# Kernel optimization log

Measured on AMD Instinct MI355X. Metric: run time of the kernel, lower is better.

## Reference

```python
import jax, jax.numpy as jnp
import numpy as np

N = 169343        # ogbn-arxiv nodes
E_DIR = 2709488   # directed edges before symmetrization (avg degree ~16)
F_IN = 128
HID = 256
C = 40
ALPHA = 0.9       # propagation matrix is I - ALPHA * S (SPD, so CG converges)
TOL = 1e-5
MAXITER = 100
EPS = 1e-5        # haiku LayerNorm default eps


def _layernorm_axis0(x, scale, offset):
    # hk.LayerNorm(0, True, True): stats over the node axis, per-feature params
    mu = jnp.mean(x, axis=0, keepdims=True)
    var = jnp.mean(jnp.square(x - mu), axis=0, keepdims=True)
    return scale * (x - mu) * jax.lax.rsqrt(var + EPS) + offset


def setup_inputs() -> dict:
    key = jax.random.key(0)
    ks = jax.random.split(key, 8)
    src = jax.random.randint(ks[0], (E_DIR,), 0, N)
    dst = jax.random.randint(ks[1], (E_DIR,), 0, N)
    # symmetrize so S is symmetric -> I - ALPHA*S is SPD
    senders = jnp.concatenate([src, dst])
    receivers = jnp.concatenate([dst, src])
    deg = jnp.maximum(jnp.zeros((N,), jnp.float32).at[receivers].add(1.0), 1.0)
    edge_weights = jax.lax.rsqrt(deg[senders] * deg[receivers])  # D^-1/2 A D^-1/2
    node_features = jax.random.normal(ks[2], (N, F_IN), jnp.float32)

    def dense(k, fin, fout):
        return jax.random.normal(k, (fin, fout), jnp.float32) / np.sqrt(fin).astype(np.float32)

    return {
        "node_features": node_features,
        "senders": senders,
        "receivers": receivers,
        "edge_weights": edge_weights,
        "W0": dense(ks[3], F_IN, HID), "b0": jnp.zeros((HID,), jnp.float32),
        "g0": jnp.ones((HID,), jnp.float32), "o0": jnp.zeros((HID,), jnp.float32),
        "W1": dense(ks[4], HID, HID), "b1": jnp.zeros((HID,), jnp.float32),
        "g1": jnp.ones((HID,), jnp.float32), "o1": jnp.zeros((HID,), jnp.float32),
        "W2": dense(ks[5], HID, C), "b2": jnp.zeros((C,), jnp.float32),
        "is_training": False,
    }


def reference(node_features, senders, receivers, edge_weights,
              W0, b0, g0, o0, W1, b1, g1, o1, W2, b2, is_training):
    # MLP stack (dropout is identity since is_training=False / eval mode)
    h = jax.nn.relu(_layernorm_axis0(node_features @ W0 + b0, g0, o0))  # [N, HID]
    h = jax.nn.relu(_layernorm_axis0(h @ W1 + b1, g1, o1))              # [N, HID]
    logits = h @ W2 + b2                                                # [N, C]

    def matvec(x):  # (I - ALPHA * S) @ x, sparse via edge list
        msg = edge_weights[:, None] * x[senders]                        # [2E, C]
        return x - ALPHA * jax.ops.segment_sum(msg, receivers, num_segments=N)

    out, _ = jax.scipy.sparse.linalg.cg(matvec, logits, tol=TOL, maxiter=MAXITER)
    return out
```

## Files before the change

kernel.cpp:

```cpp
#include <hip/hip_runtime.h>
#include <hip/hip_fp16.h>

#define FIN   128
#define HIDN  256
#define CDIM  40
#define NITER 9
#define RB    2048
#define NBSH  10
#define NBMAX 256
#define CHUNK 8192
#define BSTRIDE 36864

typedef _Float16 h8 __attribute__((ext_vector_type(8)));
typedef float f4 __attribute__((ext_vector_type(4)));


__device__ __forceinline__ float block_reduce_256(float v, float* red) {
  const int t = threadIdx.x;
  __syncthreads();
  red[t] = v;
  __syncthreads();
#pragma unroll
  for (int o = 128; o > 0; o >>= 1) {
    if (t < o) red[t] += red[t + o];
    __syncthreads();
  }
  return red[0];
}

__device__ __forceinline__ unsigned pack_half2(float a, float b) {
  __half2 h = __floats2half2_rn(a, b);
  return *reinterpret_cast<unsigned*>(&h);
}


__global__ void zero_i32(int* __restrict__ a, int n) {
  int i = blockIdx.x * blockDim.x + threadIdx.x;
  int s = gridDim.x * blockDim.x;
  for (; i < n; i += s) a[i] = 0;
}

__global__ __launch_bounds__(256) void csr_binA(
    const int* __restrict__ send, const int* __restrict__ recv,
    const float* __restrict__ ew, uint2* __restrict__ staged,
    int* __restrict__ bcnt, int nbuck, int E2) {
  __shared__ int hist[NBMAX];
  __shared__ int offs[NBMAX];
  const int tid = threadIdx.x;
  const int c0 = blockIdx.x * CHUNK;
  const int ce = min(c0 + CHUNK, E2);
  for (int j = tid; j < nbuck; j += 256) hist[j] = 0;
  __syncthreads();
  for (int e = c0 + tid; e < ce; e += 256) atomicAdd(&hist[recv[e] >> NBSH], 1);
  __syncthreads();
  for (int j = tid; j < nbuck; j += 256)
    offs[j] = hist[j] ? atomicAdd(&bcnt[j], hist[j]) : 0;
  __syncthreads();
  for (int j = tid; j < nbuck; j += 256) hist[j] = 0;
  __syncthreads();
  for (int e = c0 + tid; e < ce; e += 256) {
    int rnode = recv[e];
    int b = rnode >> NBSH;
    int p = atomicAdd(&hist[b], 1);
    int idx = offs[b] + p;
    if (idx < BSTRIDE) {
      unsigned meta = ((unsigned)(rnode & 1023) << 18) | (unsigned)send[e];
      staged[(size_t)b * BSTRIDE + idx] = make_uint2(meta, __float_as_uint(ew[e]));
    }
  }
}

__global__ __launch_bounds__(256) void csr_bucket_scan(const int* __restrict__ bcnt,
                                                       int* __restrict__ bbase,
                                                       int* __restrict__ rowp,
                                                       int nbuck, int Nn) {
  __shared__ int lb[NBMAX];
  const int tid = threadIdx.x;
  for (int j = tid; j < nbuck; j += 256) lb[j] = bcnt[j];
  __syncthreads();
  if (tid == 0) {
    int base = 0;
    for (int b = 0; b < nbuck; ++b) { int c = lb[b]; lb[b] = base; base += c; }
    rowp[Nn] = base;
  }
  __syncthreads();
  for (int j = tid; j < nbuck; j += 256) bbase[j] = lb[j];
}

__global__ __launch_bounds__(256) void csr_passB(
    const uint2* __restrict__ staged, const int* __restrict__ bcnt,
    const int* __restrict__ bbase, int* __restrict__ rowp,
    int2* __restrict__ ecsr, int Nn) {
  __shared__ int cnt[1024];
  __shared__ int part[256];
  const int tid = threadIdx.x;
  const int b = blockIdx.x;
  const int n0 = b << NBSH;
  const int nn = min(1024, Nn - n0);
  const int cntE = bcnt[b];
  const size_t sbase = (size_t)b * BSTRIDE;
  const int fbase = bbase[b];
  for (int j = tid; j < 1024; j += 256) cnt[j] = 0;
  __syncthreads();
  for (int e = tid; e < cntE; e += 256) {
    unsigned meta = staged[sbase + e].x;
    atomicAdd(&cnt[meta >> 18], 1);
  }
  __syncthreads();
  const int b4 = tid * 4;
  int c0 = cnt[b4], c1 = cnt[b4 + 1], c2 = cnt[b4 + 2], c3 = cnt[b4 + 3];
  part[tid] = c0 + c1 + c2 + c3;
  __syncthreads();
  for (int o = 1; o < 256; o <<= 1) {
    int v = (tid >= o) ? part[tid - o] : 0;
    __syncthreads();
    part[tid] += v;
    __syncthreads();
  }
  int pre = (tid == 0) ? 0 : part[tid - 1];
  cnt[b4] = pre;
  cnt[b4 + 1] = pre + c0;
  cnt[b4 + 2] = pre + c0 + c1;
  cnt[b4 + 3] = pre + c0 + c1 + c2;
  __syncthreads();
  for (int j = tid; j < nn; j += 256) rowp[n0 + j] = fbase + cnt[j];
  __syncthreads();
  for (int e = tid; e < cntE; e += 256) {
    uint2 rec = staged[sbase + e];
    int rlow = rec.x >> 18;
    int col = rec.x & 0x3FFFF;
    int pos = atomicAdd(&cnt[rlow], 1);
    ecsr[fbase + pos] = make_int2(col, (int)rec.y);
  }
}


__global__ __launch_bounds__(256) void wconv(const float* __restrict__ w0,
                                             const float* __restrict__ w1,
                                             const float* __restrict__ w2,
                                             _Float16* __restrict__ out,
                                             int n0, int n1, int n2) {
  int i = blockIdx.x * 256 + threadIdx.x;
  int s = gridDim.x * 256;
  int tot = n0 + n1 + n2;
  for (; i < tot; i += s) {
    float v = (i < n0) ? w0[i] : (i < n0 + n1) ? w1[i - n0] : w2[i - n0 - n1];
    out[i] = (_Float16)v;
  }
}


template <bool AF32, bool LNA, bool STATS, bool INITCG>
__global__ __launch_bounds__(256) void gemm_mfma(
    const void* __restrict__ Avoid, const _Float16* __restrict__ Wh,
    const float* __restrict__ bias, const float* __restrict__ lnS,
    const float* __restrict__ lnT, void* __restrict__ Cvoid,
    float* __restrict__ statp,
    float* __restrict__ rP, float* __restrict__ pP,
    __half* __restrict__ phP, float* __restrict__ xP,
    float* __restrict__ rsp,
    int M, int K, int Nn) {
  __shared__ _Float16 As[128][40];
  __shared__ _Float16 Bs[64][40];
  __shared__ _Float16 sSh[256];
  __shared__ _Float16 sTh[256];
  __shared__ float sred[4][2][64];
  __shared__ float red[256];
  const int tid = threadIdx.x;
  if (LNA) {
    if (tid < K) { sSh[tid] = (_Float16)lnS[tid]; sTh[tid] = (_Float16)lnT[tid]; }
  }
  const int w = tid >> 6, l = tid & 63;
  const int lm = l & 15;
  const int lk = (l >> 4) * 8;
  const int lr4 = (l >> 4) * 4;
  const int arow = tid >> 1, acol = (tid & 1) * 16;
  const int bn = tid & 63, bk = (tid >> 6) * 8;
  const int rowBase = blockIdx.x * 128;
  const int n0 = blockIdx.y * 64;
  const int gr = rowBase + arow;
  const int gn = n0 + bn;
  f4 acc[2][4];
#pragma unroll
  for (int mi = 0; mi < 2; ++mi)
#pragma unroll
    for (int ni = 0; ni < 4; ++ni) {
      acc[mi][ni][0] = 0.f; acc[mi][ni][1] = 0.f;
      acc[mi][ni][2] = 0.f; acc[mi][ni][3] = 0.f;
    }

  for (int k0 = 0; k0 < K; k0 += 32) {
    h8 a0, a1;
    if (gr < M) {
      if (AF32) {
        const f4* ap = reinterpret_cast<const f4*>(
            (const float*)Avoid + (size_t)gr * K + k0 + acol);
#pragma unroll
        for (int v4 = 0; v4 < 2; ++v4) {
          f4 vv = ap[v4];
#pragma unroll
          for (int j = 0; j < 4; ++j) a0[v4 * 4 + j] = (_Float16)vv[j];
        }
#pragma unroll
        for (int v4 = 2; v4 < 4; ++v4) {
          f4 vv = ap[v4];
#pragma unroll
          for (int j = 0; j < 4; ++j) a1[(v4 - 2) * 4 + j] = (_Float16)vv[j];
        }
      } else {
        const h8* ap = reinterpret_cast<const h8*>(
            (const _Float16*)Avoid + (size_t)gr * K + k0 + acol);
        a0 = ap[0];
        a1 = ap[1];
      }
    } else {
#pragma unroll
      for (int j = 0; j < 8; ++j) { a0[j] = (_Float16)0.f; a1[j] = (_Float16)0.f; }
    }
    h8 hb;
#pragma unroll
    for (int j = 0; j < 8; ++j)
      hb[j] = (gn < Nn) ? Wh[(size_t)(k0 + bk + j) * Nn + gn] : (_Float16)0.f;

    __syncthreads();
    if (LNA) {
      h8 s0 = *reinterpret_cast<const h8*>(&sSh[k0 + acol]);
      h8 s1 = *reinterpret_cast<const h8*>(&sSh[k0 + acol + 8]);
      h8 t0 = *reinterpret_cast<const h8*>(&sTh[k0 + acol]);
      h8 t1 = *reinterpret_cast<const h8*>(&sTh[k0 + acol + 8]);
      a0 = a0 * s0 + t0;
      a1 = a1 * s1 + t1;
#pragma unroll
      for (int j = 0; j < 8; ++j) {
        a0[j] = a0[j] > (_Float16)0.f ? a0[j] : (_Float16)0.f;
        a1[j] = a1[j] > (_Float16)0.f ? a1[j] : (_Float16)0.f;
      }
    }
    *reinterpret_cast<h8*>(&As[arow][acol]) = a0;
    *reinterpret_cast<h8*>(&As[arow][acol + 8]) = a1;
    *reinterpret_cast<h8*>(&Bs[bn][bk]) = hb;
    __syncthreads();

    h8 bf[4];
#pragma unroll
    for (int ni = 0; ni < 4; ++ni)
      bf[ni] = *reinterpret_cast<const h8*>(&Bs[ni * 16 + lm][lk]);
#pragma unroll
    for (int mi = 0; mi < 2; ++mi) {
      h8 af = *reinterpret_cast<const h8*>(&As[w * 32 + mi * 16 + lm][lk]);
#pragma unroll
      for (int ni = 0; ni < 4; ++ni)
        acc[mi][ni] = __builtin_amdgcn_mfma_f32_16x16x32_f16(af, bf[ni], acc[mi][ni],
                                                             0, 0, 0);
    }
  }

  float sN[4] = {0.f, 0.f, 0.f, 0.f};
  float s2N[4] = {0.f, 0.f, 0.f, 0.f};
  float rsacc = 0.f;
#pragma unroll
  for (int mi = 0; mi < 2; ++mi)
#pragma unroll
    for (int ni = 0; ni < 4; ++ni) {
      int col = n0 + ni * 16 + lm;
      if (col >= Nn) continue;
      float bb = bias[col];
#pragma unroll
      for (int r = 0; r < 4; ++r) {
        int row = rowBase + w * 32 + mi * 16 + lr4 + r;
        if (row >= M) continue;
        float v = acc[mi][ni][r] + bb;
        if (INITCG) {
          size_t idx = (size_t)row * Nn + col;
          rP[idx] = v;
          pP[idx] = v;
          xP[idx] = 0.f;
          phP[(size_t)row * 64 + col] = __float2half(v);
          rsacc = fmaf(v, v, rsacc);
        } else {
          ((_Float16*)Cvoid)[(size_t)row * Nn + col] = (_Float16)v;
        }
        if (STATS) {
          sN[ni] += v;
          s2N[ni] = fmaf(v, v, s2N[ni]);
        }
      }
    }

  if (STATS) {
#pragma unroll
    for (int ni = 0; ni < 4; ++ni) {
      sN[ni] += __shfl_xor(sN[ni], 16);
      sN[ni] += __shfl_xor(sN[ni], 32);
      s2N[ni] += __shfl_xor(s2N[ni], 16);
      s2N[ni] += __shfl_xor(s2N[ni], 32);
    }
    __syncthreads();
    if (l < 16) {
#pragma unroll
      for (int ni = 0; ni < 4; ++ni) {
        sred[w][0][ni * 16 + l] = sN[ni];
        sred[w][1][ni * 16 + l] = s2N[ni];
      }
    }
    __syncthreads();
    if (tid < 64) {
      float t0 = sred[0][0][tid] + sred[1][0][tid] + sred[2][0][tid] + sred[3][0][tid];
      float t1 = sred[0][1][tid] + sred[1][1][tid] + sred[2][1][tid] + sred[3][1][tid];
      statp[(size_t)blockIdx.x * 512 + n0 + tid] = t0;
      statp[(size_t)blockIdx.x * 512 + 256 + n0 + tid] = t1;
    }
  }

  if (INITCG) {
    for (int idx = tid; idx < 128 * 6; idx += 256) {
      int row = rowBase + idx / 6;
      int ck = idx % 6;
      if (row < M) {
        uint2* dst = reinterpret_cast<uint2*>(phP + (size_t)row * 64 + 40) + ck;
        *dst = make_uint2(0u, 0u);
      }
    }
    float bs = block_reduce_256(rsacc, red);
    if (tid == 0) rsp[blockIdx.x] = bs;
  }
}


__global__ __launch_bounds__(256) void stats_final(const float* __restrict__ part,
                                                   const float* __restrict__ g,
                                                   const float* __restrict__ o,
                                                   float* __restrict__ lnS,
                                                   float* __restrict__ lnT,
                                                   int nblk, int M) {
  __shared__ float red[256];
  const int col = blockIdx.x;
  float s = 0.f, s2 = 0.f;
  for (int b = threadIdx.x; b < nblk; b += 256) {
    s += part[(size_t)b * 512 + col];
    s2 += part[(size_t)b * 512 + 256 + col];
  }
  float ts = block_reduce_256(s, red);
  float ts2 = block_reduce_256(s2, red);
  if (threadIdx.x == 0) {
    float invM = 1.f / (float)M;
    float mean = ts * invM;
    float var = fmaxf(ts2 * invM - mean * mean, 0.f);
    float rstd = rsqrtf(var + 1e-5f);
    float sc = g[col] * rstd;
    lnS[col] = sc;
    lnT[col] = o[col] - mean * sc;
  }
}

__global__ __launch_bounds__(256) void reduce_rs(const float* __restrict__ rs_p,
                                                 float* __restrict__ rsbuf, int count) {
  __shared__ float red[256];
  float s = 0.f;
  for (int i = threadIdx.x; i < count; i += 256) s += rs_p[i];
  float t = block_reduce_256(s, red);
  if (threadIdx.x == 0) rsbuf[0] = t;
}


__global__ __launch_bounds__(256) void cg_matvec(const float* __restrict__ p,
                                                 const __half* __restrict__ ph,
                                                 float* __restrict__ q,
                                                 const int* __restrict__ rowp,
                                                 const int2* __restrict__ ecsr,
                                                 float* __restrict__ pqp,
                                                 float* __restrict__ qqp, int N) {
  __shared__ float red[256];
  const int lane = threadIdx.x & 63;
  const int wid = threadIdx.x >> 6;
  const bool act = lane < CDIM;
  float pqacc = 0.f, qqacc = 0.f;
  for (int i = blockIdx.x * 4 + wid; i < N; i += gridDim.x * 4) {
    int beg = rowp[i], end = rowp[i + 1];
    float a0 = 0.f, a1 = 0.f, a2 = 0.f, a3 = 0.f;
    int e = beg;
    for (; e + 8 <= end; e += 8) {
      int2 e0 = ecsr[e],     e1 = ecsr[e + 1], e2 = ecsr[e + 2], e3 = ecsr[e + 3];
      int2 e4 = ecsr[e + 4], e5 = ecsr[e + 5], e6 = ecsr[e + 6], e7 = ecsr[e + 7];
      if (act) {
        a0 = fmaf(__int_as_float(e0.y), __half2float(ph[(size_t)e0.x * 64 + lane]), a0);
        a1 = fmaf(__int_as_float(e1.y), __half2float(ph[(size_t)e1.x * 64 + lane]), a1);
        a2 = fmaf(__int_as_float(e2.y), __half2float(ph[(size_t)e2.x * 64 + lane]), a2);
        a3 = fmaf(__int_as_float(e3.y), __half2float(ph[(size_t)e3.x * 64 + lane]), a3);
        a0 = fmaf(__int_as_float(e4.y), __half2float(ph[(size_t)e4.x * 64 + lane]), a0);
        a1 = fmaf(__int_as_float(e5.y), __half2float(ph[(size_t)e5.x * 64 + lane]), a1);
        a2 = fmaf(__int_as_float(e6.y), __half2float(ph[(size_t)e6.x * 64 + lane]), a2);
        a3 = fmaf(__int_as_float(e7.y), __half2float(ph[(size_t)e7.x * 64 + lane]), a3);
      }
    }
    for (; e + 4 <= end; e += 4) {
      int2 e0 = ecsr[e], e1 = ecsr[e + 1], e2 = ecsr[e + 2], e3 = ecsr[e + 3];
      if (act) {
        a0 = fmaf(__int_as_float(e0.y), __half2float(ph[(size_t)e0.x * 64 + lane]), a0);
        a1 = fmaf(__int_as_float(e1.y), __half2float(ph[(size_t)e1.x * 64 + lane]), a1);
        a2 = fmaf(__int_as_float(e2.y), __half2float(ph[(size_t)e2.x * 64 + lane]), a2);
        a3 = fmaf(__int_as_float(e3.y), __half2float(ph[(size_t)e3.x * 64 + lane]), a3);
      }
    }
    for (; e < end; ++e) {
      int2 e0 = ecsr[e];
      if (act)
        a0 = fmaf(__int_as_float(e0.y), __half2float(ph[(size_t)e0.x * 64 + lane]), a0);
    }
    if (act) {
      float pvv = p[(size_t)i * CDIM + lane];
      float qvv = fmaf(-0.9f, (a0 + a1) + (a2 + a3), pvv);
      q[(size_t)i * CDIM + lane] = qvv;
      pqacc = fmaf(pvv, qvv, pqacc);
      qqacc = fmaf(qvv, qvv, qqacc);
    }
  }
  float s1 = block_reduce_256(pqacc, red);
  float s2 = block_reduce_256(qqacc, red);
  if (threadIdx.x == 0) { pqp[blockIdx.x] = s1; qqp[blockIdx.x] = s2; }
}

__global__ __launch_bounds__(256) void cg_fused(float4* __restrict__ x,
                                                float4* __restrict__ r,
                                                float4* __restrict__ p,
                                                const float4* __restrict__ q,
                                                __half* __restrict__ ph,
                                                const float* __restrict__ pqp,
                                                const float* __restrict__ qqp,
                                                const float* __restrict__ rs_in,
                                                float* __restrict__ rs_out, int total4) {
  __shared__ float red[256];
  float s1 = 0.f, s2 = 0.f;
  for (int i = threadIdx.x; i < RB; i += 256) {
    s1 += pqp[i];
    s2 += qqp[i];
  }
  float pq = block_reduce_256(s1, red);
  float qq = block_reduce_256(s2, red);
  float rsold = *rs_in;
  float alpha = (pq > 0.f) ? (rsold / pq) : 0.f;
  float rsnew = fmaxf(fmaf(alpha * alpha, qq, -rsold), 0.f);
  float beta = (rsold > 0.f) ? (rsnew / rsold) : 0.f;
  if (threadIdx.x == 0) *rs_out = rsnew;
  for (int j = blockIdx.x * 256 + threadIdx.x; j < total4; j += gridDim.x * 256) {
    const int node = j / 10;
    const int qx = j - node * 10;
    float4 pv4 = p[j], qv4 = q[j], xv4 = x[j], rv4 = r[j];
    xv4.x = fmaf(alpha, pv4.x, xv4.x);
    xv4.y = fmaf(alpha, pv4.y, xv4.y);
    xv4.z = fmaf(alpha, pv4.z, xv4.z);
    xv4.w = fmaf(alpha, pv4.w, xv4.w);
    rv4.x = fmaf(-alpha, qv4.x, rv4.x);
    rv4.y = fmaf(-alpha, qv4.y, rv4.y);
    rv4.z = fmaf(-alpha, qv4.z, rv4.z);
    rv4.w = fmaf(-alpha, qv4.w, rv4.w);
    float4 pn;
    pn.x = fmaf(beta, pv4.x, rv4.x);
    pn.y = fmaf(beta, pv4.y, rv4.y);
    pn.z = fmaf(beta, pv4.z, rv4.z);
    pn.w = fmaf(beta, pv4.w, rv4.w);
    x[j] = xv4;
    r[j] = rv4;
    p[j] = pn;
    unsigned* dst = reinterpret_cast<unsigned*>(ph + (size_t)node * 64 + qx * 4);
    dst[0] = pack_half2(pn.x, pn.y);
    dst[1] = pack_half2(pn.z, pn.w);
  }
}


extern "C" void kernel_launch(void* const* d_in, const int* in_sizes, int n_in,
                              void* d_out, int out_size, void* d_ws, size_t ws_size,
                              hipStream_t stream) {
  const float* X   = (const float*)d_in[0];
  const int* send  = (const int*)d_in[1];
  const int* recv  = (const int*)d_in[2];
  const float* ew  = (const float*)d_in[3];
  const float* W0  = (const float*)d_in[4];
  const float* b0  = (const float*)d_in[5];
  const float* g0  = (const float*)d_in[6];
  const float* o0  = (const float*)d_in[7];
  const float* W1  = (const float*)d_in[8];
  const float* b1  = (const float*)d_in[9];
  const float* g1  = (const float*)d_in[10];
  const float* o1  = (const float*)d_in[11];
  const float* W2  = (const float*)d_in[12];
  const float* b2  = (const float*)d_in[13];

  const int N = in_sizes[0] / FIN;
  const int E2 = in_sizes[1];
  const int total = N * CDIM;
  const int total4 = total / 4;
  const int gm = (N + 127) / 128;
  const int nbuck = (N + 1023) >> NBSH;
  const int nw0 = FIN * HIDN, nw1 = HIDN * HIDN, nw2 = HIDN * CDIM;

  char* base = (char*)d_ws;
  size_t off = 0;
  auto carve = [&](size_t bytes) -> void* {
    void* ptr = base + off;
    off += (bytes + 255) & ~(size_t)255;
    return ptr;
  };
  int* rowp      = (int*)carve((size_t)(N + 1) * 4);
  int2* ecsr     = (int2*)carve((size_t)E2 * 8);
  _Float16* Y0h  = (_Float16*)carve((size_t)N * HIDN * 2);
  _Float16* Y1h  = (_Float16*)carve((size_t)N * HIDN * 2);
  float* statp   = (float*)carve((size_t)gm * 512 * 4);
  float* lnS0    = (float*)carve(256 * 4);
  float* lnT0    = (float*)carve(256 * 4);
  float* lnS1    = (float*)carve(256 * 4);
  float* lnT1    = (float*)carve(256 * 4);
  float* pqp     = (float*)carve((size_t)RB * 4);
  float* qqp     = (float*)carve((size_t)RB * 4);
  float* rsp     = (float*)carve((size_t)gm * 4);
  float* rsbuf   = (float*)carve(2 * 4);
  int* bcnt      = (int*)carve((size_t)nbuck * 4);
  int* bbase     = (int*)carve((size_t)nbuck * 4);
  _Float16* Whb  = (_Float16*)carve((size_t)(nw0 + nw1 + nw2) * 2);
  (void)n_in; (void)out_size;

  if (off > ws_size) return;
  if (nbuck > NBMAX) return;

  _Float16* Wh0 = Whb;
  _Float16* Wh1 = Whb + nw0;
  _Float16* Wh2 = Whb + nw0 + nw1;

  uint2* staged = (uint2*)Y0h;
  float* rv = (float*)Y0h;
  float* pv = rv + (size_t)total;
  float* qv = rv + (size_t)2 * total;
  __half* ph = (__half*)Y1h;
  float* xv = (float*)d_out;

  zero_i32<<<1, 256, 0, stream>>>(bcnt, nbuck);
  wconv<<<64, 256, 0, stream>>>(W0, W1, W2, Whb, nw0, nw1, nw2);
  const int nchunk = (E2 + CHUNK - 1) / CHUNK;
  csr_binA<<<nchunk, 256, 0, stream>>>(send, recv, ew, staged, bcnt, nbuck, E2);
  csr_bucket_scan<<<1, 256, 0, stream>>>(bcnt, bbase, rowp, nbuck, N);
  csr_passB<<<nbuck, 256, 0, stream>>>(staged, bcnt, bbase, rowp, ecsr, N);

  gemm_mfma<true, false, true, false><<<dim3(gm, HIDN / 64), 256, 0, stream>>>(
      X, Wh0, b0, nullptr, nullptr, Y0h, statp,
      nullptr, nullptr, nullptr, nullptr, nullptr, N, FIN, HIDN);
  stats_final<<<HIDN, 256, 0, stream>>>(statp, g0, o0, lnS0, lnT0, gm, N);
  gemm_mfma<false, true, true, false><<<dim3(gm, HIDN / 64), 256, 0, stream>>>(
      Y0h, Wh1, b1, lnS0, lnT0, Y1h, statp,
      nullptr, nullptr, nullptr, nullptr, nullptr, N, HIDN, HIDN);
  stats_final<<<HIDN, 256, 0, stream>>>(statp, g1, o1, lnS1, lnT1, gm, N);
  gemm_mfma<false, true, false, true><<<dim3(gm, 1), 256, 0, stream>>>(
      Y1h, Wh2, b2, lnS1, lnT1, nullptr, nullptr,
      rv, pv, ph, xv, rsp, N, HIDN, CDIM);
  reduce_rs<<<1, 256, 0, stream>>>(rsp, rsbuf, gm);

  for (int it = 0; it < NITER; ++it) {
    cg_matvec<<<RB, 256, 0, stream>>>(pv, ph, qv, rowp, ecsr, pqp, qqp, N);
    cg_fused<<<RB, 256, 0, stream>>>((float4*)xv, (float4*)rv, (float4*)pv,
                                     (const float4*)qv, ph, pqp, qqp,
                                     &rsbuf[it & 1], &rsbuf[(it + 1) & 1], total4);
  }
}
```

Baseline: 2.077 ms.

## Split half-precision search direction into 32+8 planes and drop fp32 p copy

The CG direction vector p is no longer kept in fp32. Only an fp16 copy remains, and it is stored as two compact arrays: 32 columns per row and 8 columns per row, replacing the padded 64-wide layout. The matvec gathers read 80 bytes per node instead of touching 128-byte padded rows, and the fused update no longer reads and writes an fp32 p. This also removes the padding-zero stores. The catch is that p is now kept only in fp16, so the x and beta updates use rounded p, which may loosen CG accuracy.

```diff
diff --git a/kernel.cpp b/kernel.cpp
--- a/kernel.cpp
+++ b/kernel.cpp
@@ -156,8 +156,8 @@
     const float* __restrict__ bias, const float* __restrict__ lnS,
     const float* __restrict__ lnT, void* __restrict__ Cvoid,
     float* __restrict__ statp,
-    float* __restrict__ rP, float* __restrict__ pP,
-    __half* __restrict__ phP, float* __restrict__ xP,
+    float* __restrict__ rP, __half* __restrict__ ph32P,
+    __half* __restrict__ ph8P, float* __restrict__ xP,
     float* __restrict__ rsp,
     int M, int K, int Nn) {
   __shared__ _Float16 As[128][40];
@@ -273,9 +273,9 @@
         if (INITCG) {
           size_t idx = (size_t)row * Nn + col;
           rP[idx] = v;
-          pP[idx] = v;
           xP[idx] = 0.f;
-          phP[(size_t)row * 64 + col] = __float2half(v);
+          if (col < 32) ph32P[(size_t)row * 32 + col] = __float2half(v);
+          else          ph8P[(size_t)row * 8 + col - 32] = __float2half(v);
           rsacc = fmaf(v, v, rsacc);
         } else {
           ((_Float16*)Cvoid)[(size_t)row * Nn + col] = (_Float16)v;
@@ -313,14 +313,6 @@
   }
 
   if (INITCG) {
-    for (int idx = tid; idx < 128 * 6; idx += 256) {
-      int row = rowBase + idx / 6;
-      int ck = idx % 6;
-      if (row < M) {
-        uint2* dst = reinterpret_cast<uint2*>(phP + (size_t)row * 64 + 40) + ck;
-        *dst = make_uint2(0u, 0u);
-      }
-    }
     float bs = block_reduce_256(rsacc, red);
     if (tid == 0) rsp[blockIdx.x] = bs;
   }
@@ -363,8 +355,8 @@
 }
 
 
-__global__ __launch_bounds__(256) void cg_matvec(const float* __restrict__ p,
-                                                 const __half* __restrict__ ph,
+__global__ __launch_bounds__(256) void cg_matvec(const __half* __restrict__ ph32,
+                                                 const __half* __restrict__ ph8,
                                                  float* __restrict__ q,
                                                  const int* __restrict__ rowp,
                                                  const int2* __restrict__ ecsr,
@@ -374,6 +366,8 @@
   const int lane = threadIdx.x & 63;
   const int wid = threadIdx.x >> 6;
   const bool act = lane < CDIM;
+  const __half* gb = (lane < 32) ? ph32 : (ph8 - 32);
+  const size_t gs = (lane < 32) ? 32 : 8;
   float pqacc = 0.f, qqacc = 0.f;
   for (int i = blockIdx.x * 4 + wid; i < N; i += gridDim.x * 4) {
     int beg = rowp[i], end = rowp[i + 1];
@@ -383,32 +377,32 @@
       int2 e0 = ecsr[e],     e1 = ecsr[e + 1], e2 = ecsr[e + 2], e3 = ecsr[e + 3];
       int2 e4 = ecsr[e + 4], e5 = ecsr[e + 5], e6 = ecsr[e + 6], e7 = ecsr[e + 7];
       if (act) {
-        a0 = fmaf(__int_as_float(e0.y), __half2float(ph[(size_t)e0.x * 64 + lane]), a0);
-        a1 = fmaf(__int_as_float(e1.y), __half2float(ph[(size_t)e1.x * 64 + lane]), a1);
-        a2 = fmaf(__int_as_float(e2.y), __half2float(ph[(size_t)e2.x * 64 + lane]), a2);
-        a3 = fmaf(__int_as_float(e3.y), __half2float(ph[(size_t)e3.x * 64 + lane]), a3);
-        a0 = fmaf(__int_as_float(e4.y), __half2float(ph[(size_t)e4.x * 64 + lane]), a0);
-        a1 = fmaf(__int_as_float(e5.y), __half2float(ph[(size_t)e5.x * 64 + lane]), a1);
-        a2 = fmaf(__int_as_float(e6.y), __half2float(ph[(size_t)e6.x * 64 + lane]), a2);
-        a3 = fmaf(__int_as_float(e7.y), __half2float(ph[(size_t)e7.x * 64 + lane]), a3);
+        a0 = fmaf(__int_as_float(e0.y), __half2float(gb[(size_t)e0.x * gs + lane]), a0);
+        a1 = fmaf(__int_as_float(e1.y), __half2float(gb[(size_t)e1.x * gs + lane]), a1);
+        a2 = fmaf(__int_as_float(e2.y), __half2float(gb[(size_t)e2.x * gs + lane]), a2);
+        a3 = fmaf(__int_as_float(e3.y), __half2float(gb[(size_t)e3.x * gs + lane]), a3);
+        a0 = fmaf(__int_as_float(e4.y), __half2float(gb[(size_t)e4.x * gs + lane]), a0);
+        a1 = fmaf(__int_as_float(e5.y), __half2float(gb[(size_t)e5.x * gs + lane]), a1);
+        a2 = fmaf(__int_as_float(e6.y), __half2float(gb[(size_t)e6.x * gs + lane]), a2);
+        a3 = fmaf(__int_as_float(e7.y), __half2float(gb[(size_t)e7.x * gs + lane]), a3);
       }
     }
     for (; e + 4 <= end; e += 4) {
       int2 e0 = ecsr[e], e1 = ecsr[e + 1], e2 = ecsr[e + 2], e3 = ecsr[e + 3];
       if (act) {
-        a0 = fmaf(__int_as_float(e0.y), __half2float(ph[(size_t)e0.x * 64 + lane]), a0);
-        a1 = fmaf(__int_as_float(e1.y), __half2float(ph[(size_t)e1.x * 64 + lane]), a1);
-        a2 = fmaf(__int_as_float(e2.y), __half2float(ph[(size_t)e2.x * 64 + lane]), a2);
-        a3 = fmaf(__int_as_float(e3.y), __half2float(ph[(size_t)e3.x * 64 + lane]), a3);
+        a0 = fmaf(__int_as_float(e0.y), __half2float(gb[(size_t)e0.x * gs + lane]), a0);
+        a1 = fmaf(__int_as_float(e1.y), __half2float(gb[(size_t)e1.x * gs + lane]), a1);
+        a2 = fmaf(__int_as_float(e2.y), __half2float(gb[(size_t)e2.x * gs + lane]), a2);
+        a3 = fmaf(__int_as_float(e3.y), __half2float(gb[(size_t)e3.x * gs + lane]), a3);
       }
     }
     for (; e < end; ++e) {
       int2 e0 = ecsr[e];
       if (act)
-        a0 = fmaf(__int_as_float(e0.y), __half2float(ph[(size_t)e0.x * 64 + lane]), a0);
+        a0 = fmaf(__int_as_float(e0.y), __half2float(gb[(size_t)e0.x * gs + lane]), a0);
     }
     if (act) {
-      float pvv = p[(size_t)i * CDIM + lane];
+      float pvv = __half2float(gb[(size_t)i * gs + lane]);
       float qvv = fmaf(-0.9f, (a0 + a1) + (a2 + a3), pvv);
       q[(size_t)i * CDIM + lane] = qvv;
       pqacc = fmaf(pvv, qvv, pqacc);
@@ -422,9 +416,9 @@
 
 __global__ __launch_bounds__(256) void cg_fused(float4* __restrict__ x,
                                                 float4* __restrict__ r,
-                                                float4* __restrict__ p,
                                                 const float4* __restrict__ q,
-                                                __half* __restrict__ ph,
+                                                __half* __restrict__ ph32,
+                                                __half* __restrict__ ph8,
                                                 const float* __restrict__ pqp,
                                                 const float* __restrict__ qqp,
                                                 const float* __restrict__ rs_in,
@@ -445,26 +439,33 @@
   for (int j = blockIdx.x * 256 + threadIdx.x; j < total4; j += gridDim.x * 256) {
     const int node = j / 10;
     const int qx = j - node * 10;
-    float4 pv4 = p[j], qv4 = q[j], xv4 = x[j], rv4 = r[j];
-    xv4.x = fmaf(alpha, pv4.x, xv4.x);
-    xv4.y = fmaf(alpha, pv4.y, xv4.y);
-    xv4.z = fmaf(alpha, pv4.z, xv4.z);
-    xv4.w = fmaf(alpha, pv4.w, xv4.w);
+    __half* pb = (qx < 8) ? (ph32 + (size_t)node * 32 + qx * 4)
+                          : (ph8 + (size_t)node * 8 + (qx - 8) * 4);
+    union { uint2 u; __half h[4]; } uu;
+    uu.u = *reinterpret_cast<const uint2*>(pb);
+    float p0 = __half2float(uu.h[0]);
+    float p1 = __half2float(uu.h[1]);
+    float p2 = __half2float(uu.h[2]);
+    float p3 = __half2float(uu.h[3]);
+    float4 qv4 = q[j], xv4 = x[j], rv4 = r[j];
+    xv4.x = fmaf(alpha, p0, xv4.x);
+    xv4.y = fmaf(alpha, p1, xv4.y);
+    xv4.z = fmaf(alpha, p2, xv4.z);
+    xv4.w = fmaf(alpha, p3, xv4.w);
     rv4.x = fmaf(-alpha, qv4.x, rv4.x);
     rv4.y = fmaf(-alpha, qv4.y, rv4.y);
     rv4.z = fmaf(-alpha, qv4.z, rv4.z);
     rv4.w = fmaf(-alpha, qv4.w, rv4.w);
-    float4 pn;
-    pn.x = fmaf(beta, pv4.x, rv4.x);
-    pn.y = fmaf(beta, pv4.y, rv4.y);
-    pn.z = fmaf(beta, pv4.z, rv4.z);
-    pn.w = fmaf(beta, pv4.w, rv4.w);
+    float n0 = fmaf(beta, p0, rv4.x);
+    float n1 = fmaf(beta, p1, rv4.y);
+    float n2 = fmaf(beta, p2, rv4.z);
+    float n3 = fmaf(beta, p3, rv4.w);
     x[j] = xv4;
     r[j] = rv4;
-    p[j] = pn;
-    unsigned* dst = reinterpret_cast<unsigned*>(ph + (size_t)node * 64 + qx * 4);
-    dst[0] = pack_half2(pn.x, pn.y);
-    dst[1] = pack_half2(pn.z, pn.w);
+    uint2 out;
+    out.x = pack_half2(n0, n1);
+    out.y = pack_half2(n2, n3);
+    *reinterpret_cast<uint2*>(pb) = out;
   }
 }
 
@@ -529,9 +530,9 @@
 
   uint2* staged = (uint2*)Y0h;
   float* rv = (float*)Y0h;
-  float* pv = rv + (size_t)total;
-  float* qv = rv + (size_t)2 * total;
-  __half* ph = (__half*)Y1h;
+  float* qv = rv + (size_t)total;
+  __half* ph32 = (__half*)Y1h;
+  __half* ph8 = (__half*)Y1h + (size_t)N * 32;
   float* xv = (float*)d_out;
 
   zero_i32<<<1, 256, 0, stream>>>(bcnt, nbuck);
@@ -551,13 +552,13 @@
   stats_final<<<HIDN, 256, 0, stream>>>(statp, g1, o1, lnS1, lnT1, gm, N);
   gemm_mfma<false, true, false, true><<<dim3(gm, 1), 256, 0, stream>>>(
       Y1h, Wh2, b2, lnS1, lnT1, nullptr, nullptr,
-      rv, pv, ph, xv, rsp, N, HIDN, CDIM);
+      rv, ph32, ph8, xv, rsp, N, HIDN, CDIM);
   reduce_rs<<<1, 256, 0, stream>>>(rsp, rsbuf, gm);
 
   for (int it = 0; it < NITER; ++it) {
-    cg_matvec<<<RB, 256, 0, stream>>>(pv, ph, qv, rowp, ecsr, pqp, qqp, N);
-    cg_fused<<<RB, 256, 0, stream>>>((float4*)xv, (float4*)rv, (float4*)pv,
-                                     (const float4*)qv, ph, pqp, qqp,
+    cg_matvec<<<RB, 256, 0, stream>>>(ph32, ph8, qv, rowp, ecsr, pqp, qqp, N);
+    cg_fused<<<RB, 256, 0, stream>>>((float4*)xv, (float4*)rv, (const float4*)qv,
+                                     ph32, ph8, pqp, qqp,
                                      &rsbuf[it & 1], &rsbuf[(it + 1) & 1], total4);
   }
 }
```

After: 2.059 ms. About the same (-0.8%).
